# Optimization experiments

Hardware: AMD Instinct MI355X
Metric: run time of the kernel (lower is better)

Reference implementation:

```python
import jax, jax.numpy as jnp
import numpy as np

N = 50000
E = 800000
D = 64
UNITS = 128


def _linear_params(key, fan_in, fan_out):
    k1, k2 = jax.random.split(key)
    bound = 1.0 / np.sqrt(fan_in)
    W = jax.random.uniform(k1, (fan_in, fan_out), minval=-bound, maxval=bound, dtype=jnp.float32)
    b = jax.random.uniform(k2, (fan_out,), minval=-bound, maxval=bound, dtype=jnp.float32)
    return W, b


def setup_inputs() -> dict:
    key = jax.random.key(0)
    ks = jax.random.split(key, 7)
    x = jax.random.normal(ks[0], (N, D), dtype=jnp.float32)
    edge_tensor = jax.random.randint(ks[1], (2, E), 0, N, dtype=jnp.int64)
    W1, b1 = _linear_params(ks[2], D, 2 * D)
    W2, b2 = _linear_params(ks[3], 2 * D, 4 * D)
    W3, b3 = _linear_params(ks[4], 4 * D, UNITS)
    W4, b4 = _linear_params(ks[5], UNITS, UNITS)
    W5, b5 = _linear_params(ks[6], UNITS, 1)
    return {"x": x, "edge_tensor": edge_tensor,
            "W1": W1, "b1": b1, "W2": W2, "b2": b2, "W3": W3, "b3": b3,
            "W4": W4, "b4": b4, "W5": W5, "b5": b5}


def _gin_conv(h, src, dst, W, b):
    # GINConv with default eps=0: MLP((1+eps)*x_i + sum_{j in N(i)} x_j)
    msgs = h[src]                                    # [E, d] gather
    agg = jax.ops.segment_sum(msgs, dst, num_segments=N)  # [N, d] scatter-add
    return jax.nn.relu((agg + h) @ W + b)


def reference(x, edge_tensor, W1, b1, W2, b2, W3, b3, W4, b4, W5, b5):
    src = edge_tensor[0]
    dst = edge_tensor[1]
    h = _gin_conv(x, src, dst, W1, b1)   # [N, 2D]
    h = _gin_conv(h, src, dst, W2, b2)   # [N, 4D]
    h = jax.nn.relu(h @ W3 + b3)         # [N, units]
    h = jax.nn.relu(h @ W4 + b4)         # [N, units]
    return h @ W5 + b5                   # [N, 1]
```

## Files before the change

kernel.cpp:

```cpp
#include <hip/hip_runtime.h>
#include <cstddef>

#define N_NODES 50000
#define N_EDGES 800000

__global__ void zero_int_kernel(int* __restrict__ p, int n) {
    int stride = gridDim.x * blockDim.x;
    for (int i = blockIdx.x * blockDim.x + threadIdx.x; i < n; i += stride) p[i] = 0;
}

__global__ void hist_kernel(const int* __restrict__ dst, int* __restrict__ deg, int E) {
    int stride = gridDim.x * blockDim.x;
    for (int e = blockIdx.x * blockDim.x + threadIdx.x; e < E; e += stride)
        atomicAdd(&deg[dst[e]], 1);
}

__global__ __launch_bounds__(1024)
void scan_kernel(const int* __restrict__ deg, int* __restrict__ row_ptr,
                 int* __restrict__ cursor, int n) {
    __shared__ int wsum[16];
    __shared__ int carry_s;
    const int lane = threadIdx.x & 63;
    const int wid  = threadIdx.x >> 6;
    if (threadIdx.x == 0) carry_s = 0;
    __syncthreads();
    for (int base = 0; base < n; base += 1024) {
        int i = base + threadIdx.x;
        int v = (i < n) ? deg[i] : 0;
        int s = v;
#pragma unroll
        for (int off = 1; off < 64; off <<= 1) {
            int t = __shfl_up(s, off, 64);
            if (lane >= off) s += t;
        }
        if (lane == 63) wsum[wid] = s;
        __syncthreads();
        if (wid == 0) {
            int ws = (lane < 16) ? wsum[lane] : 0;
#pragma unroll
            for (int off = 1; off < 16; off <<= 1) {
                int t = __shfl_up(ws, off, 64);
                if (lane >= off) ws += t;
            }
            if (lane < 16) wsum[lane] = ws;
        }
        __syncthreads();
        int carry = carry_s;
        int wave_off = wid ? wsum[wid - 1] : 0;
        int excl = carry + wave_off + s - v;
        if (i < n) { row_ptr[i] = excl; cursor[i] = excl; }
        __syncthreads();
        if (threadIdx.x == 1023) carry_s = carry + wsum[15];
        __syncthreads();
    }
    if (threadIdx.x == 0) row_ptr[n] = carry_s;
}

__global__ void fill_kernel(const int* __restrict__ src, const int* __restrict__ dst,
                            int* __restrict__ cursor, int* __restrict__ col, int E) {
    int stride = gridDim.x * blockDim.x;
    for (int e = blockIdx.x * blockDim.x + threadIdx.x; e < E; e += stride) {
        int p = atomicAdd(&cursor[dst[e]], 1);
        col[p] = src[e];
    }
}

template<int D>
__global__ __launch_bounds__(256)
void gin_aggregate(const float* __restrict__ feat, const int* __restrict__ row_ptr,
                   const int* __restrict__ col, float* __restrict__ agg, int n) {
    int gwid = (blockIdx.x * blockDim.x + threadIdx.x) >> 6;
    int lane = threadIdx.x & 63;
    int nwav = (gridDim.x * blockDim.x) >> 6;
    for (int v = gwid; v < n; v += nwav) {
        float2 acc;
        if constexpr (D == 128) acc = ((const float2*)(feat + (size_t)v * D))[lane];
        else { acc.x = feat[(size_t)v * D + lane]; acc.y = 0.f; }
        int beg = row_ptr[v], end = row_ptr[v + 1];
        for (int j = beg; j < end; j += 64) {
            int batch = end - j; if (batch > 64) batch = 64;
            int e = (lane < batch) ? col[j + lane] : 0;
            for (int k = 0; k < batch; ++k) {
                int s = __shfl(e, k, 64);
                if constexpr (D == 128) {
                    float2 r = ((const float2*)(feat + (size_t)s * D))[lane];
                    acc.x += r.x; acc.y += r.y;
                } else {
                    acc.x += feat[(size_t)s * D + lane];
                }
            }
        }
        if constexpr (D == 128) ((float2*)(agg + (size_t)v * D))[lane] = acc;
        else agg[(size_t)v * D + lane] = acc.x;
    }
}

__global__ __launch_bounds__(256)
void gemm_bias_relu(const float* __restrict__ A, const float* __restrict__ W,
                    const float* __restrict__ bias, float* __restrict__ C,
                    int M, int K, int N, int do_relu) {
    __shared__ __align__(16) float As[16][68];
    __shared__ __align__(16) float Bs[16][68];

    const int tid = threadIdx.x;
    const int tx  = tid & 15;
    const int ty  = tid >> 4;
    const int row0 = blockIdx.y * 64;
    const int col0 = blockIdx.x * 64;

    float acc[4][4];
#pragma unroll
    for (int i = 0; i < 4; ++i)
#pragma unroll
        for (int j = 0; j < 4; ++j) acc[i][j] = 0.f;

    const int am = tid >> 2;
    const int ak = (tid & 3) << 2;
    int arow = row0 + am;
    if (arow >= M) arow = M - 1;
    const int bk = tid >> 4;
    const int bn = (tid & 15) << 2;

    for (int k0 = 0; k0 < K; k0 += 16) {
        float4 av = *(const float4*)(A + (size_t)arow * K + k0 + ak);
        float4 bv = *(const float4*)(W + (size_t)(k0 + bk) * N + col0 + bn);
        As[ak + 0][am] = av.x;
        As[ak + 1][am] = av.y;
        As[ak + 2][am] = av.z;
        As[ak + 3][am] = av.w;
        *(float4*)(&Bs[bk][bn]) = bv;
        __syncthreads();
#pragma unroll
        for (int kk = 0; kk < 16; ++kk) {
            float4 a4 = *(const float4*)(&As[kk][ty << 2]);
            float4 b4 = *(const float4*)(&Bs[kk][tx << 2]);
            float a[4] = {a4.x, a4.y, a4.z, a4.w};
            float b[4] = {b4.x, b4.y, b4.z, b4.w};
#pragma unroll
            for (int i = 0; i < 4; ++i)
#pragma unroll
                for (int j = 0; j < 4; ++j)
                    acc[i][j] = fmaf(a[i], b[j], acc[i][j]);
        }
        __syncthreads();
    }

    float4 bb = *(const float4*)(bias + col0 + (tx << 2));
    float bias4[4] = {bb.x, bb.y, bb.z, bb.w};
#pragma unroll
    for (int i = 0; i < 4; ++i) {
        int row = row0 + (ty << 2) + i;
        if (row < M) {
            float4 v;
            float* vp = &v.x;
#pragma unroll
            for (int j = 0; j < 4; ++j) {
                float t = acc[i][j] + bias4[j];
                if (do_relu) t = fmaxf(t, 0.f);
                vp[j] = t;
            }
            *(float4*)(C + (size_t)row * N + col0 + (tx << 2)) = v;
        }
    }
}

__global__ void out_proj_kernel(const float* __restrict__ h, const float* __restrict__ w,
                                const float* __restrict__ b, float* __restrict__ out, int M) {
    int lane = threadIdx.x & 63;
    int wave = threadIdx.x >> 6;
    int wpb  = blockDim.x >> 6;
    float w0 = w[lane], w1 = w[64 + lane];
    float bb = b[0];
    for (int row = blockIdx.x * wpb + wave; row < M; row += gridDim.x * wpb) {
        const float* hr = h + (size_t)row * 128;
        float s = hr[lane] * w0 + hr[64 + lane] * w1;
#pragma unroll
        for (int off = 32; off > 0; off >>= 1) s += __shfl_xor(s, off, 64);
        if (lane == 0) out[row] = s + bb;
    }
}

extern "C" void kernel_launch(void* const* d_in, const int* in_sizes, int n_in,
                              void* d_out, int out_size, void* d_ws, size_t ws_size,
                              hipStream_t stream) {
    const float* x    = (const float*)d_in[0];
    const int*   edge = (const int*)d_in[1];
    const float* W1 = (const float*)d_in[2];
    const float* b1 = (const float*)d_in[3];
    const float* W2 = (const float*)d_in[4];
    const float* b2 = (const float*)d_in[5];
    const float* W3 = (const float*)d_in[6];
    const float* b3 = (const float*)d_in[7];
    const float* W4 = (const float*)d_in[8];
    const float* b4 = (const float*)d_in[9];
    const float* W5 = (const float*)d_in[10];
    const float* b5 = (const float*)d_in[11];
    float* out = (float*)d_out;

    const int N = N_NODES, E = N_EDGES;
    const int* src = edge;
    const int* dst = edge + E;

    float* ws   = (float*)d_ws;
    float* h1   = ws;
    float* agg1 = ws + (size_t)N * 128;
    float* agg2 = ws + (size_t)N * 256;
    float* h2   = ws;
    float* h3   = ws + (size_t)N * 256;
    float* h4   = ws;

    int* ibase   = (int*)(ws + (size_t)N * 384);
    int* deg     = ibase;
    int* row_ptr = ibase + N;
    int* colidx  = ibase + 2 * N + 1;

    dim3 blk(256);

    zero_int_kernel<<<64, blk, 0, stream>>>(deg, N);
    hist_kernel<<<2048, blk, 0, stream>>>(dst, deg, E);
    scan_kernel<<<1, 1024, 0, stream>>>(deg, row_ptr, deg, N);
    fill_kernel<<<2048, blk, 0, stream>>>(src, dst, deg, colidx, E);

    gin_aggregate<64><<<3125, blk, 0, stream>>>(x, row_ptr, colidx, agg1, N);
    dim3 g1(128 / 64, (N + 63) / 64);
    gemm_bias_relu<<<g1, blk, 0, stream>>>(agg1, W1, b1, h1, N, 64, 128, 1);

    gin_aggregate<128><<<3125, blk, 0, stream>>>(h1, row_ptr, colidx, agg2, N);
    dim3 g2(256 / 64, (N + 63) / 64);
    gemm_bias_relu<<<g2, blk, 0, stream>>>(agg2, W2, b2, h2, N, 128, 256, 1);

    dim3 g3(128 / 64, (N + 63) / 64);
    gemm_bias_relu<<<g3, blk, 0, stream>>>(h2, W3, b3, h3, N, 256, 128, 1);
    gemm_bias_relu<<<g3, blk, 0, stream>>>(h3, W4, b4, h4, N, 128, 128, 1);
    out_proj_kernel<<<2048, blk, 0, stream>>>(h4, W5, b5, out, N);
}
```

Baseline: 501.6 us.

## Parallelize CSR prefix scan across blocks and enlarge GEMM register tiles

Replaces the single-block serial prefix scan over node degrees with a three-kernel multi-block scan: per-block scans, a scan of the block totals, then an add pass. This removes a long single-workgroup loop over 49 chunks. The GEMM is also templated to 128-row tiles with 8xTN outputs per thread (TN of 4 or 8) for more register reuse per shared-memory load. The cost is two extra launches, extra workspace for the per-block partials, and higher register pressure in the GEMM.

Measured after the change: 460.9 us. 1.09x faster.

```diff
diff --git a/kernel.cpp b/kernel.cpp
--- a/kernel.cpp
+++ b/kernel.cpp
@@ -16,44 +16,59 @@
 }
 
 __global__ __launch_bounds__(1024)
-void scan_kernel(const int* __restrict__ deg, int* __restrict__ row_ptr,
-                 int* __restrict__ cursor, int n) {
+void scan_blocks(const int* __restrict__ deg, int* __restrict__ loc,
+                 int* __restrict__ part, int n) {
     __shared__ int wsum[16];
-    __shared__ int carry_s;
     const int lane = threadIdx.x & 63;
     const int wid  = threadIdx.x >> 6;
-    if (threadIdx.x == 0) carry_s = 0;
+    int i = blockIdx.x * 1024 + threadIdx.x;
+    int v = (i < n) ? deg[i] : 0;
+    int s = v;
+#pragma unroll
+    for (int off = 1; off < 64; off <<= 1) {
+        int t = __shfl_up(s, off, 64);
+        if (lane >= off) s += t;
+    }
+    if (lane == 63) wsum[wid] = s;
     __syncthreads();
-    for (int base = 0; base < n; base += 1024) {
-        int i = base + threadIdx.x;
-        int v = (i < n) ? deg[i] : 0;
-        int s = v;
-#pragma unroll
-        for (int off = 1; off < 64; off <<= 1) {
-            int t = __shfl_up(s, off, 64);
-            if (lane >= off) s += t;
-        }
-        if (lane == 63) wsum[wid] = s;
-        __syncthreads();
-        if (wid == 0) {
-            int ws = (lane < 16) ? wsum[lane] : 0;
-#pragma unroll
-            for (int off = 1; off < 16; off <<= 1) {
-                int t = __shfl_up(ws, off, 64);
-                if (lane >= off) ws += t;
-            }
-            if (lane < 16) wsum[lane] = ws;
-        }
-        __syncthreads();
-        int carry = carry_s;
-        int wave_off = wid ? wsum[wid - 1] : 0;
-        int excl = carry + wave_off + s - v;
-        if (i < n) { row_ptr[i] = excl; cursor[i] = excl; }
-        __syncthreads();
-        if (threadIdx.x == 1023) carry_s = carry + wsum[15];
-        __syncthreads();
-    }
-    if (threadIdx.x == 0) row_ptr[n] = carry_s;
+    if (wid == 0) {
+        int ws = (lane < 16) ? wsum[lane] : 0;
+#pragma unroll
+        for (int off = 1; off < 16; off <<= 1) {
+            int t = __shfl_up(ws, off, 64);
+            if (lane >= off) ws += t;
+        }
+        if (lane < 16) wsum[lane] = ws;
+    }
+    __syncthreads();
+    int excl = (wid ? wsum[wid - 1] : 0) + s - v;
+    if (i < n) loc[i] = excl;
+    if (threadIdx.x == 1023) part[blockIdx.x] = wsum[15];
+}
+
+__global__ void scan_tops(int* __restrict__ part, int nb) {
+    int lane = threadIdx.x;
+    int v = (lane < nb) ? part[lane] : 0;
+    int s = v;
+#pragma unroll
+    for (int off = 1; off < 64; off <<= 1) {
+        int t = __shfl_up(s, off, 64);
+        if (lane >= off) s += t;
+    }
+    if (lane < nb) part[lane] = s - v;
+    if (lane == nb - 1) part[nb] = s;
+}
+
+__global__ __launch_bounds__(1024)
+void scan_add(const int* __restrict__ loc, const int* __restrict__ part,
+              int* __restrict__ row_ptr, int* __restrict__ cursor, int n, int nb) {
+    int i = blockIdx.x * 1024 + threadIdx.x;
+    if (i < n) {
+        int r = loc[i] + part[i >> 10];
+        row_ptr[i] = r;
+        cursor[i]  = r;
+    }
+    if (i == 0) row_ptr[n] = part[nb];
 }
 
 __global__ void fill_kernel(const int* __restrict__ src, const int* __restrict__ dst,
@@ -95,71 +110,100 @@
     }
 }
 
+template<int BN>
 __global__ __launch_bounds__(256)
 void gemm_bias_relu(const float* __restrict__ A, const float* __restrict__ W,
                     const float* __restrict__ bias, float* __restrict__ C,
                     int M, int K, int N, int do_relu) {
-    __shared__ __align__(16) float As[16][68];
-    __shared__ __align__(16) float Bs[16][68];
+    constexpr int TN = BN / 16;
+    __shared__ __align__(16) float As[16][132];
+    __shared__ __align__(16) float Bs[16][BN + 4];
 
     const int tid = threadIdx.x;
     const int tx  = tid & 15;
     const int ty  = tid >> 4;
-    const int row0 = blockIdx.y * 64;
-    const int col0 = blockIdx.x * 64;
-
-    float acc[4][4];
-#pragma unroll
-    for (int i = 0; i < 4; ++i)
-#pragma unroll
-        for (int j = 0; j < 4; ++j) acc[i][j] = 0.f;
-
-    const int am = tid >> 2;
-    const int ak = (tid & 3) << 2;
-    int arow = row0 + am;
-    if (arow >= M) arow = M - 1;
-    const int bk = tid >> 4;
-    const int bn = (tid & 15) << 2;
+    const int row0 = blockIdx.y * 128;
+    const int col0 = blockIdx.x * BN;
+
+    float acc[8][TN];
+#pragma unroll
+    for (int i = 0; i < 8; ++i)
+#pragma unroll
+        for (int j = 0; j < TN; ++j) acc[i][j] = 0.f;
+
+    constexpr int BF4   = BN / 4;
+    constexpr int BLOAD = 16 * BF4 / 256;
 
     for (int k0 = 0; k0 < K; k0 += 16) {
-        float4 av = *(const float4*)(A + (size_t)arow * K + k0 + ak);
-        float4 bv = *(const float4*)(W + (size_t)(k0 + bk) * N + col0 + bn);
-        As[ak + 0][am] = av.x;
-        As[ak + 1][am] = av.y;
-        As[ak + 2][am] = av.z;
-        As[ak + 3][am] = av.w;
-        *(float4*)(&Bs[bk][bn]) = bv;
+#pragma unroll
+        for (int h = 0; h < 2; ++h) {
+            int idx = tid + h * 256;
+            int ar  = idx >> 2;
+            int akc = (idx & 3) << 2;
+            int arow = row0 + ar; if (arow >= M) arow = M - 1;
+            float4 av = *(const float4*)(A + (size_t)arow * K + k0 + akc);
+            As[akc + 0][ar] = av.x;
+            As[akc + 1][ar] = av.y;
+            As[akc + 2][ar] = av.z;
+            As[akc + 3][ar] = av.w;
+        }
+#pragma unroll
+        for (int h = 0; h < BLOAD; ++h) {
+            int idx = tid + h * 256;
+            int kr  = idx / BF4;
+            int cc  = (idx % BF4) << 2;
+            float4 bv = *(const float4*)(W + (size_t)(k0 + kr) * N + col0 + cc);
+            *(float4*)(&Bs[kr][cc]) = bv;
+        }
         __syncthreads();
 #pragma unroll
         for (int kk = 0; kk < 16; ++kk) {
-            float4 a4 = *(const float4*)(&As[kk][ty << 2]);
-            float4 b4 = *(const float4*)(&Bs[kk][tx << 2]);
-            float a[4] = {a4.x, a4.y, a4.z, a4.w};
-            float b[4] = {b4.x, b4.y, b4.z, b4.w};
-#pragma unroll
-            for (int i = 0; i < 4; ++i)
-#pragma unroll
-                for (int j = 0; j < 4; ++j)
+            float a[8];
+            float4 a0 = *(const float4*)(&As[kk][ty << 2]);
+            float4 a1 = *(const float4*)(&As[kk][64 + (ty << 2)]);
+            a[0]=a0.x; a[1]=a0.y; a[2]=a0.z; a[3]=a0.w;
+            a[4]=a1.x; a[5]=a1.y; a[6]=a1.z; a[7]=a1.w;
+            float b[TN];
+            float4 b0 = *(const float4*)(&Bs[kk][tx << 2]);
+            b[0]=b0.x; b[1]=b0.y; b[2]=b0.z; b[3]=b0.w;
+            if constexpr (TN == 8) {
+                float4 b1 = *(const float4*)(&Bs[kk][64 + (tx << 2)]);
+                b[4]=b1.x; b[5]=b1.y; b[6]=b1.z; b[7]=b1.w;
+            }
+#pragma unroll
+            for (int i = 0; i < 8; ++i)
+#pragma unroll
+                for (int j = 0; j < TN; ++j)
                     acc[i][j] = fmaf(a[i], b[j], acc[i][j]);
         }
         __syncthreads();
     }
 
-    float4 bb = *(const float4*)(bias + col0 + (tx << 2));
-    float bias4[4] = {bb.x, bb.y, bb.z, bb.w};
-#pragma unroll
-    for (int i = 0; i < 4; ++i) {
-        int row = row0 + (ty << 2) + i;
+    float bs[TN];
+    {
+        float4 bb0 = *(const float4*)(bias + col0 + (tx << 2));
+        bs[0]=bb0.x; bs[1]=bb0.y; bs[2]=bb0.z; bs[3]=bb0.w;
+        if constexpr (TN == 8) {
+            float4 bb1 = *(const float4*)(bias + col0 + 64 + (tx << 2));
+            bs[4]=bb1.x; bs[5]=bb1.y; bs[6]=bb1.z; bs[7]=bb1.w;
+        }
+    }
+#pragma unroll
+    for (int i = 0; i < 8; ++i) {
+        int row = row0 + ((i < 4) ? (ty << 2) + i : 64 + (ty << 2) + (i - 4));
         if (row < M) {
-            float4 v;
-            float* vp = &v.x;
-#pragma unroll
-            for (int j = 0; j < 4; ++j) {
-                float t = acc[i][j] + bias4[j];
-                if (do_relu) t = fmaxf(t, 0.f);
-                vp[j] = t;
+#pragma unroll
+            for (int g = 0; g < TN / 4; ++g) {
+                float4 v;
+                float* vp = &v.x;
+#pragma unroll
+                for (int j = 0; j < 4; ++j) {
+                    float t = acc[i][g * 4 + j] + bs[g * 4 + j];
+                    if (do_relu) t = fmaxf(t, 0.f);
+                    vp[j] = t;
+                }
+                *(float4*)(C + (size_t)row * N + col0 + g * 64 + (tx << 2)) = v;
             }
-            *(float4*)(C + (size_t)row * N + col0 + (tx << 2)) = v;
         }
     }
 }
@@ -213,24 +257,27 @@
     int* deg     = ibase;
     int* row_ptr = ibase + N;
     int* colidx  = ibase + 2 * N + 1;
+    int* loc     = ibase + 2 * N + 1 + E;
+    int* part    = loc + N;
+
+    const int NB = (N + 1023) / 1024;
 
     dim3 blk(256);
 
     zero_int_kernel<<<64, blk, 0, stream>>>(deg, N);
     hist_kernel<<<2048, blk, 0, stream>>>(dst, deg, E);
-    scan_kernel<<<1, 1024, 0, stream>>>(deg, row_ptr, deg, N);
+    scan_blocks<<<NB, 1024, 0, stream>>>(deg, loc, part, N);
+    scan_tops<<<1, 64, 0, stream>>>(part, NB);
+    scan_add<<<NB, 1024, 0, stream>>>(loc, part, row_ptr, deg, N, NB);
     fill_kernel<<<2048, blk, 0, stream>>>(src, dst, deg, colidx, E);
 
     gin_aggregate<64><<<3125, blk, 0, stream>>>(x, row_ptr, colidx, agg1, N);
-    dim3 g1(128 / 64, (N + 63) / 64);
-    gemm_bias_relu<<<g1, blk, 0, stream>>>(agg1, W1, b1, h1, N, 64, 128, 1);
+    gemm_bias_relu<64><<<dim3(2, 391), blk, 0, stream>>>(agg1, W1, b1, h1, N, 64, 128, 1);
 
     gin_aggregate<128><<<3125, blk, 0, stream>>>(h1, row_ptr, colidx, agg2, N);
-    dim3 g2(256 / 64, (N + 63) / 64);
-    gemm_bias_relu<<<g2, blk, 0, stream>>>(agg2, W2, b2, h2, N, 128, 256, 1);
-
-    dim3 g3(128 / 64, (N + 63) / 64);
-    gemm_bias_relu<<<g3, blk, 0, stream>>>(h2, W3, b3, h3, N, 256, 128, 1);
-    gemm_bias_relu<<<g3, blk, 0, stream>>>(h3, W4, b4, h4, N, 128, 128, 1);
+    gemm_bias_relu<128><<<dim3(2, 391), blk, 0, stream>>>(agg2, W2, b2, h2, N, 128, 256, 1);
+
+    gemm_bias_relu<64><<<dim3(2, 391), blk, 0, stream>>>(h2, W3, b3, h3, N, 256, 128, 1);
+    gemm_bias_relu<64><<<dim3(2, 391), blk, 0, stream>>>(h3, W4, b4, h4, N, 128, 128, 1);
     out_proj_kernel<<<2048, blk, 0, stream>>>(h4, W5, b5, out, N);
 }
```
